# Kernel optimization log

Hardware: AMD Instinct MI355X
Metric: run time of the kernel (lower is better)

Reference implementation:

```python
import jax, jax.numpy as jnp
import numpy as np

EPS = float(np.finfo(np.float32).eps)

# (joint_id, joint_name, parent_name) in the module's fkm_computation_order
ORDER = [
    (1, 'rHip', 'hip'), (2, 'rKnee', 'rHip'), (3, 'rAnkle', 'rKnee'), (4, 'rToe', 'rAnkle'),
    (6, 'lHip', 'hip'), (7, 'lKnee', 'lHip'), (8, 'lAnkle', 'lKnee'), (9, 'lToe', 'lAnkle'),
    (11, 'spine', 'hip'), (12, 'spine1', 'spine'), (13, 'thorax', 'spine1'), (14, 'neck', 'thorax'),
    (15, 'head', 'neck'), (16, 'lShoulderAnchor', 'spine1'), (17, 'lShoulder', 'lShoulderAnchor'),
    (18, 'lElbow', 'lShoulder'), (19, 'lWrist', 'lElbow'), (20, 'lThumb', 'lWrist'),
    (22, 'lWristEnd', 'lWrist'), (24, 'rShoulderAnchor', 'spine1'), (25, 'rShoulder', 'rShoulderAnchor'),
    (26, 'rElbow', 'rShoulder'), (27, 'rWrist', 'rElbow'), (28, 'rThumb', 'rWrist'),
    (30, 'rWristEnd', 'rWrist'),
]


def axis_angle_to_matrix(a):
    """Rodrigues formula, batched. a: [B,3] -> [B,3,3]."""
    theta = jnp.linalg.norm(a, axis=-1, keepdims=True)  # [B,1]
    r = a / (theta + EPS)                               # [B,3]
    r0, r1, r2 = r[:, 0], r[:, 1], r[:, 2]
    z = jnp.zeros_like(r0)
    # skew-symmetric S with S[0,1]=-r2, S[0,2]=r1, S[1,2]=-r0 (as in torch code)
    S = jnp.stack([
        jnp.stack([z, -r2, r1], axis=-1),
        jnp.stack([r2, z, -r0], axis=-1),
        jnp.stack([-r1, r0, z], axis=-1),
    ], axis=-2)  # [B,3,3]
    th = theta[..., None]  # [B,1,1]
    I = jnp.eye(3, dtype=a.dtype)
    return I + jnp.sin(th) * S + (1.0 - jnp.cos(th)) * (S @ S)


def setup_inputs() -> dict:
    key = jax.random.key(0)
    k1, k2 = jax.random.split(key)
    B = 262144
    x = jax.random.normal(k1, (B, 99), dtype=jnp.float32)
    offset = jax.random.normal(k2, (32, 3), dtype=jnp.float32)
    return {"x": x, "offset": offset}


def reference(x, offset):
    # hip root: position from first 3 dims, orientation from dims 3:6
    pos = {"hip": offset[0] + x[:, 0:3]}                # [B,3]
    ang = {"hip": axis_angle_to_matrix(x[:, 3:6])}      # [B,3,3]
    # local rotations for every joint in the chain: dims [3*id+3 : 3*id+6]
    local = {name: axis_angle_to_matrix(x[:, 3 * i + 3: 3 * i + 6]) for i, name, _ in ORDER}
    # sequential forward kinematics down the tree
    for i, cur, par in ORDER:
        # offset[i] @ R_parent  (row-vector times matrix), then translate
        pos[cur] = jnp.einsum('j,bjk->bk', offset[i], ang[par]) + pos[par]
        ang[cur] = local[cur] @ ang[par]
    # positions in the same order as get_joint_positions(): hip then chain order
    return jnp.stack([pos['hip']] + [pos[c] for _, c, _ in ORDER], axis=1)  # [B,26,3]
```

## Files before the change

kernel.cpp:

```cpp
#include <hip/hip_runtime.h>

#define TPB  256
#define RPW  64
#define XDIM 99
#define NJ   26
#define OUTW 78

constexpr int OFF_IDX[NJ] = {0,1,2,3,4,6,7,8,9,11,12,13,14,15,16,17,18,19,20,22,24,25,26,27,28,30};
constexpr int PAR[NJ]     = {-1,0,1,2,3,0,5,6,7,0,9,10,11,12,10,14,15,16,17,17,10,20,21,22,23,23};

__device__ __forceinline__ float fast_rcp(float a)  { return __builtin_amdgcn_rcpf(a); }
__device__ __forceinline__ float fast_sqrt(float a) { return __builtin_amdgcn_sqrtf(a); }

__device__ __forceinline__ void rodrigues(float ax, float ay, float az, float* R) {
    const float EPS = 1.1920928955078125e-07f;
    float t = fast_sqrt(ax*ax + ay*ay + az*az);
    float inv = fast_rcp(t + EPS);
    float r0 = ax*inv, r1 = ay*inv, r2 = az*inv;
    float s, c;
    __sincosf(t, &s, &c);
    float omc = 1.0f - c;
    float r00 = r0*r0, r11 = r1*r1, r22 = r2*r2;
    float r01 = r0*r1, r02 = r0*r2, r12 = r1*r2;
    R[0] = 1.0f - omc*(r11 + r22);
    R[1] = -s*r2 + omc*r01;
    R[2] =  s*r1 + omc*r02;
    R[3] =  s*r2 + omc*r01;
    R[4] = 1.0f - omc*(r00 + r22);
    R[5] = -s*r0 + omc*r12;
    R[6] = -s*r1 + omc*r02;
    R[7] =  s*r0 + omc*r12;
    R[8] = 1.0f - omc*(r00 + r11);
}

#define STEP(s) do {                                                          \
    const int i_  = OFF_IDX[(s)];                                             \
    const int pa_ = PAR[(s)];                                                 \
    float L[9];                                                               \
    rodrigues(row[3*i_+3], row[3*i_+4], row[3*i_+5], L);                      \
    const float o0 = off[3*i_], o1 = off[3*i_+1], o2 = off[3*i_+2];           \
    _Pragma("unroll")                                                         \
    for (int c = 0; c < 3; ++c)                                               \
        pp[(s)][c] = o0*ang[pa_][c] + o1*ang[pa_][3+c] + o2*ang[pa_][6+c]     \
                   + pp[pa_][c];                                              \
    _Pragma("unroll")                                                         \
    for (int j = 0; j < 3; ++j)                                               \
        _Pragma("unroll")                                                     \
        for (int kk = 0; kk < 3; ++kk)                                        \
            ang[(s)][3*j+kk] = L[3*j+0]*ang[pa_][0+kk]                        \
                             + L[3*j+1]*ang[pa_][3+kk]                        \
                             + L[3*j+2]*ang[pa_][6+kk];                       \
} while (0)

__global__ __launch_bounds__(TPB, 4) void skel_fk(const float* __restrict__ x,
                                                  const float* __restrict__ off,
                                                  float* __restrict__ out) {
    __shared__ __align__(16) float buf[RPW * XDIM];
    const int t = threadIdx.x;
    const int w = t >> 6;
    const int l = t & 63;
    const int row0 = blockIdx.x * RPW;
    const float* gsrc = x + (long long)row0 * XDIM;

    #pragma unroll
    for (int j = 0; j < 6; ++j) {
        const int jj = 6 * w + j;
        __builtin_amdgcn_global_load_lds(
            (const __attribute__((address_space(1))) unsigned int*)(gsrc + 256*jj + 4*l),
            (__attribute__((address_space(3))) unsigned int*)(buf + 256*jj),
            16, 0, 0);
    }
    if (w >= 1) {
        const int kk = w - 1;
        __builtin_amdgcn_global_load_lds(
            (const __attribute__((address_space(1))) unsigned int*)(gsrc + 6144 + 64*kk + l),
            (__attribute__((address_space(3))) unsigned int*)(buf + 6144 + 64*kk),
            4, 0, 0);
    }
    __syncthreads();

    const float* row = &buf[l * XDIM];
    float ang[NJ][9];
    float pp[NJ][3];

    {
        float R[9];
        rodrigues(row[3], row[4], row[5], R);
        #pragma unroll
        for (int q = 0; q < 9; ++q) ang[0][q] = R[q];
        pp[0][0] = off[0] + row[0];
        pp[0][1] = off[1] + row[1];
        pp[0][2] = off[2] + row[2];
    }

    if (w == 0) {
        #pragma unroll
        for (int s = 1; s <= 8; ++s) STEP(s);
    } else if (w == 1) {
        #pragma unroll
        for (int s = 9; s <= 13; ++s) STEP(s);
    } else if (w == 2) {
        STEP(9); STEP(10);
        #pragma unroll
        for (int s = 14; s <= 19; ++s) STEP(s);
    } else {
        STEP(9); STEP(10);
        #pragma unroll
        for (int s = 20; s <= 25; ++s) STEP(s);
    }
    __syncthreads();

    {
        float* srow = &buf[l * OUTW];
        if (w == 0) {
            #pragma unroll
            for (int s = 1; s <= 8; ++s) {
                srow[3*s+0] = pp[s][0]; srow[3*s+1] = pp[s][1]; srow[3*s+2] = pp[s][2];
            }
        } else if (w == 1) {
            srow[0] = pp[0][0]; srow[1] = pp[0][1]; srow[2] = pp[0][2];
            #pragma unroll
            for (int s = 9; s <= 13; ++s) {
                srow[3*s+0] = pp[s][0]; srow[3*s+1] = pp[s][1]; srow[3*s+2] = pp[s][2];
            }
        } else if (w == 2) {
            #pragma unroll
            for (int s = 14; s <= 19; ++s) {
                srow[3*s+0] = pp[s][0]; srow[3*s+1] = pp[s][1]; srow[3*s+2] = pp[s][2];
            }
        } else {
            #pragma unroll
            for (int s = 20; s <= 25; ++s) {
                srow[3*s+0] = pp[s][0]; srow[3*s+1] = pp[s][1]; srow[3*s+2] = pp[s][2];
            }
        }
    }
    __syncthreads();

    {
        float4* ob4 = reinterpret_cast<float4*>(out + (long long)row0 * OUTW);
        const float4* b4 = reinterpret_cast<const float4*>(buf);
        #pragma unroll
        for (int j = 0; j < 4; ++j)
            ob4[t + 256*j] = b4[t + 256*j];
        if (t < 224) ob4[1024 + t] = b4[1024 + t];
    }
}

extern "C" void kernel_launch(void* const* d_in, const int* in_sizes, int n_in,
                              void* d_out, int out_size, void* d_ws, size_t ws_size,
                              hipStream_t stream) {
    const float* x   = (const float*)d_in[0];
    const float* off = (const float*)d_in[1];
    float* out = (float*)d_out;
    const int B = in_sizes[0] / XDIM;
    const int grid = B / RPW;
    skel_fk<<<grid, TPB, 0, stream>>>(x, off, out);
}
```

Measured before the change: 36.77 us.

## Process two row slabs per block with upfront double-buffered LDS DMA

Each block now handles two 64-row slabs. It issues the global-to-LDS loads for both slabs at the start, then uses partial vmcnt waits and raw barriers so the second slab's load overlaps the first slab's compute and store. The goal is to hide load latency inside a block and halve the grid size. In exchange, LDS per block doubles and the occupancy hint drops from 4 to 3 blocks. Correctness now depends on hand-counted vmcnt values that must also account for the interleaved global stores.

```diff
diff --git a/kernel.cpp b/kernel.cpp
--- a/kernel.cpp
+++ b/kernel.cpp
@@ -1,10 +1,11 @@
 #include <hip/hip_runtime.h>
 
 #define TPB  256
-#define RPW  64
+#define RPS  64
 #define XDIM 99
 #define NJ   26
 #define OUTW 78
+#define SLABF (RPS * XDIM)
 
 constexpr int OFF_IDX[NJ] = {0,1,2,3,4,6,7,8,9,11,12,13,14,15,16,17,18,19,20,22,24,25,26,27,28,30};
 constexpr int PAR[NJ]     = {-1,0,1,2,3,0,5,6,7,0,9,10,11,12,10,14,15,16,17,17,10,20,21,22,23,23};
@@ -52,34 +53,28 @@
                              + L[3*j+2]*ang[pa_][6+kk];                       \
 } while (0)
 
-__global__ __launch_bounds__(TPB, 4) void skel_fk(const float* __restrict__ x,
-                                                  const float* __restrict__ off,
-                                                  float* __restrict__ out) {
-    __shared__ __align__(16) float buf[RPW * XDIM];
-    const int t = threadIdx.x;
-    const int w = t >> 6;
-    const int l = t & 63;
-    const int row0 = blockIdx.x * RPW;
-    const float* gsrc = x + (long long)row0 * XDIM;
-
+__device__ __forceinline__ void dma_slab(const float* gsrc, float* lbuf, int w, int l) {
     #pragma unroll
     for (int j = 0; j < 6; ++j) {
         const int jj = 6 * w + j;
         __builtin_amdgcn_global_load_lds(
             (const __attribute__((address_space(1))) unsigned int*)(gsrc + 256*jj + 4*l),
-            (__attribute__((address_space(3))) unsigned int*)(buf + 256*jj),
+            (__attribute__((address_space(3))) unsigned int*)(lbuf + 256*jj),
             16, 0, 0);
     }
     if (w >= 1) {
         const int kk = w - 1;
         __builtin_amdgcn_global_load_lds(
             (const __attribute__((address_space(1))) unsigned int*)(gsrc + 6144 + 64*kk + l),
-            (__attribute__((address_space(3))) unsigned int*)(buf + 6144 + 64*kk),
+            (__attribute__((address_space(3))) unsigned int*)(lbuf + 6144 + 64*kk),
             4, 0, 0);
     }
-    __syncthreads();
+}
 
-    const float* row = &buf[l * XDIM];
+__device__ __forceinline__ void process_slab(float* slab, float* ob,
+                                             const float* __restrict__ off,
+                                             int t, int w, int l) {
+    const float* row = &slab[l * XDIM];
     float ang[NJ][9];
     float pp[NJ][3];
 
@@ -92,7 +87,6 @@
         pp[0][1] = off[1] + row[1];
         pp[0][2] = off[2] + row[2];
     }
-
     if (w == 0) {
         #pragma unroll
         for (int s = 1; s <= 8; ++s) STEP(s);
@@ -108,10 +102,12 @@
         #pragma unroll
         for (int s = 20; s <= 25; ++s) STEP(s);
     }
-    __syncthreads();
+
+    asm volatile("s_waitcnt lgkmcnt(0)" ::: "memory");
+    __builtin_amdgcn_s_barrier();
 
     {
-        float* srow = &buf[l * OUTW];
+        float* srow = &slab[l * OUTW];
         if (w == 0) {
             #pragma unroll
             for (int s = 1; s <= 8; ++s) {
@@ -135,16 +131,44 @@
             }
         }
     }
-    __syncthreads();
+    asm volatile("s_waitcnt lgkmcnt(0)" ::: "memory");
+    __builtin_amdgcn_s_barrier();
 
     {
-        float4* ob4 = reinterpret_cast<float4*>(out + (long long)row0 * OUTW);
-        const float4* b4 = reinterpret_cast<const float4*>(buf);
+        float4* ob4 = reinterpret_cast<float4*>(ob);
+        const float4* b4 = reinterpret_cast<const float4*>(slab);
         #pragma unroll
         for (int j = 0; j < 4; ++j)
             ob4[t + 256*j] = b4[t + 256*j];
         if (t < 224) ob4[1024 + t] = b4[1024 + t];
     }
+}
+
+__global__ __launch_bounds__(TPB, 3) void skel_fk(const float* __restrict__ x,
+                                                  const float* __restrict__ off,
+                                                  float* __restrict__ out) {
+    __shared__ __align__(16) float buf[2][SLABF];
+    const int t = threadIdx.x;
+    const int w = t >> 6;
+    const int l = t & 63;
+    const int row0 = blockIdx.x * (2 * RPS);
+    const float* gA = x + (long long)row0 * XDIM;
+    const float* gB = gA + SLABF;
+    float* oA = out + (long long)row0 * OUTW;
+    float* oB = oA + RPS * OUTW;
+
+    dma_slab(gA, buf[0], w, l);
+    dma_slab(gB, buf[1], w, l);
+
+    asm volatile("s_waitcnt vmcnt(6)" ::: "memory");
+    __builtin_amdgcn_s_barrier();
+
+    process_slab(buf[0], oA, off, t, w, l);
+
+    asm volatile("s_waitcnt vmcnt(5)" ::: "memory");
+    __builtin_amdgcn_s_barrier();
+
+    process_slab(buf[1], oB, off, t, w, l);
 }
 
 extern "C" void kernel_launch(void* const* d_in, const int* in_sizes, int n_in,
@@ -154,6 +178,6 @@
     const float* off = (const float*)d_in[1];
     float* out = (float*)d_out;
     const int B = in_sizes[0] / XDIM;
-    const int grid = B / RPW;
+    const int grid = B / (2 * RPS);
     skel_fk<<<grid, TPB, 0, stream>>>(x, off, out);
 }
```

Result: slower. 37.79 us (+2.8%).
